# Optimization experiments

Hardware: AMD Instinct MI355X
Metric: run time of the kernel (lower is better)

Reference implementation:

```python
import jax, jax.numpy as jnp
import numpy as np

# Original torch code does the CZT in float64/complex128 explicitly; match it.
jax.config.update("jax_enable_x64", True)

SR = 44100
HOP = 512
MAX_NHAR = 128
REL_WIN = 4
F0_MIN = 40.0  # reconstruction of get_n_fft(): lowest analyzable pitch
N_MAX = int(round(SR / F0_MIN * REL_WIN / 2) * 2)          # 4410: max window size
N_FFT = int(2 ** np.ceil(np.log2(N_MAX)))                  # 8192: used only for padding
L = int(2 ** np.ceil(np.log2(N_MAX + MAX_NHAR - 1)))       # 8192: Bluestein conv length (exact for all frames since L >= n_i + m_i - 1)
N_FRAMES = 1024


def setup_inputs() -> dict:
    key = jax.random.key(0)
    k1, k2 = jax.random.split(key)
    t = N_FRAMES * HOP
    x = jax.random.normal(k1, (t,), dtype=jnp.float32)
    # pitch contour in a realistic 100..400 Hz voice range
    f0 = 100.0 + 300.0 * jax.random.uniform(k2, (N_FRAMES,), dtype=jnp.float32)
    return {"x": x, "f0": f0}


def _sinusoidal_analysis_czt(x, f0):
    # f0: (F,). Vectorized, padded/masked version of the per-frame CZT loop.
    f0 = jnp.clip(f0.astype(jnp.float64), F0_MIN, None)
    F = f0.shape[0]
    nhar = jnp.minimum(jnp.floor(SR / f0 / 2.0), float(MAX_NHAR)).astype(jnp.int32)      # (F,)
    winsize = (jnp.round(SR / f0 * REL_WIN / 2.0) * 2).astype(jnp.int32)                 # (F,) even, <= N_MAX
    pad = N_FFT // 2
    x_pad = jnp.pad(x.astype(jnp.float64), (pad, pad))

    j = jnp.arange(N_MAX)
    start = jnp.arange(F) * HOP + pad                                                    # (F,)
    idx = start[:, None] - winsize[:, None] // 2 + j[None, :]                            # (F, N_MAX)
    frames = x_pad[jnp.clip(idx, 0, x_pad.shape[0] - 1)]
    # torch.blackman_window(n) is periodic: denominator = n
    ratio = j[None, :].astype(jnp.float64) / winsize[:, None].astype(jnp.float64)
    win = 0.42 - 0.5 * jnp.cos(2.0 * np.pi * ratio) + 0.08 * jnp.cos(4.0 * np.pi * ratio)
    valid = j[None, :] < winsize[:, None]
    xw = jnp.where(valid, frames * win, 0.0)                                             # (F, N_MAX) windowed frame, zero-padded

    theta = 2.0 * np.pi * f0 / SR                                                        # (F,) A=exp(+i th), W=exp(-i th)
    jj = j.astype(jnp.float64)
    # gn[j] = x[j] * A^{-j} * W^{j^2/2} = x[j] * exp(-i th (j + j^2/2))
    gphase = -theta[:, None] * (jj[None, :] + 0.5 * jj[None, :] ** 2)
    gn = jnp.zeros((F, L), dtype=jnp.complex128).at[:, :N_MAX].set(xw * jnp.exp(1j * gphase))
    # hn[k] = 1/w[k] = exp(+i th k^2/2) for k < m ; hn[L-j] = exp(+i th j^2/2) for 1 <= j < n
    # (filled for the max ranges; extra entries are never reached because gn is zero beyond winsize)
    kk = jnp.arange(L)
    off = jnp.where(kk < MAX_NHAR, kk, jnp.where(kk > L - N_MAX, L - kk, 0)).astype(jnp.float64)
    hmask = (kk < MAX_NHAR) | (kk > L - N_MAX)
    hn = jnp.where(hmask[None, :], jnp.exp(1j * theta[:, None] * 0.5 * off[None, :] ** 2), 0.0 + 0.0j)
    qn = jnp.fft.ifft(jnp.fft.fft(gn, axis=-1) * jnp.fft.fft(hn, axis=-1), axis=-1)      # (F, L)

    m = jnp.arange(MAX_NHAR).astype(jnp.float64)
    wq = jnp.exp(-1j * theta[:, None] * 0.5 * m[None, :] ** 2)                           # w[:m]
    yn = qn[:, :MAX_NHAR] * wq                                                           # (F, MAX_NHAR)
    yn = 2.381 * yn / (winsize[:, None] // 2 + 1).astype(jnp.float64)
    har_mask = m[None, :] < nhar[:, None].astype(jnp.float64)
    ampl = jnp.where(har_mask, jnp.abs(yn), 0.0).T.astype(jnp.float32)                   # (MAX_NHAR, F)
    phase = jnp.where(har_mask, jnp.angle(yn), 0.0).T.astype(jnp.float32)
    return ampl, phase


def reference(x, f0):
    return _sinusoidal_analysis_czt(x, f0)
```

## Files before the change

kernel.cpp:

```cpp
#include <hip/hip_runtime.h>

#define HOP 512
#define MAX_NHAR 128
#define N_MAX 4410
#define SEGS 8
#define CHUNK_MAX 552
#define PI_D 3.14159265358979323846

__device__ __forceinline__ void frame_params(double f0v, int& w, int& nhar, double& theta) {
    double f0d = f0v < 40.0 ? 40.0 : f0v;
    const double inv = 44100.0 / f0d;
    nhar = (int)fmin(floor(inv * 0.5), 128.0);
    w = 2 * (int)rint(inv * 2.0);
    if (w > N_MAX) w = N_MAX;
    theta = (2.0 * PI_D * f0d) / 44100.0;
}

__device__ __forceinline__ int chunk8_of(int w) {
    return (((w + SEGS - 1) / SEGS) + 7) & ~7;
}

__global__ __launch_bounds__(128) void prep_kernel(
    const float* __restrict__ f0, double* __restrict__ ccos, int F)
{
    const int f = blockIdx.x, k = threadIdx.x;
    int w, nhar; double theta;
    frame_params((double)f0[f], w, nhar, theta);
    ccos[f * MAX_NHAR + k] = cos(theta * (double)(k + 1));
}

__global__ __launch_bounds__(64) void goertzel_kernel(
    const float* __restrict__ x, const float* __restrict__ f0,
    const double* __restrict__ ccos, double2* __restrict__ parts,
    int t, int F)
{
    __shared__ double sm[CHUNK_MAX];
    const int frame = blockIdx.x >> 3;
    const int seg   = blockIdx.x & (SEGS - 1);
    const int lane  = threadIdx.x;

    int w, nhar; double theta;
    frame_params((double)f0[frame], w, nhar, theta);
    const int chunk = chunk8_of(w);
    const int j0 = seg * chunk;
    int lenp = 0;
    if (j0 < w) {
        const int l = w - j0;
        lenp = (l > chunk) ? chunk : ((l + 7) & ~7);
    }

    {
        const double c2pi_invw = (2.0 * PI_D) / (double)w;
        const int base = frame * HOP - (w >> 1) + j0;
        for (int j = lane; j < lenp; j += 64) {
            double outv = 0.0;
            if (j0 + j < w) {
                const int ix = base + j;
                const double val = (ix >= 0 && ix < t) ? (double)x[ix] : 0.0;
                const double c1 = cos(c2pi_invw * (double)(j0 + j));
                const double win = fma(0.16, c1 * c1, 0.34) - 0.5 * c1;
                outv = val * win;
            }
            sm[j] = outv;
        }
    }
    __syncthreads();

    const double Ca = 2.0 * ccos[frame * MAX_NHAR + lane];
    const double Cb = 2.0 * ccos[frame * MAX_NHAR + lane + 64];
    double s1a = 0.0, s2a = 0.0, s1b = 0.0, s2b = 0.0;

    if (nhar > 64) {
        for (int jb = 0; jb < lenp; jb += 8) {
            double xv[8];
            #pragma unroll
            for (int u = 0; u < 8; ++u) xv[u] = sm[jb + u];
            #pragma unroll
            for (int u = 0; u < 8; ++u) {
                const double ta = xv[u] - s2a;
                const double tb = xv[u] - s2b;
                const double na = fma(Ca, s1a, ta);
                const double nb = fma(Cb, s1b, tb);
                s2a = s1a; s1a = na;
                s2b = s1b; s1b = nb;
            }
        }
    } else {
        for (int jb = 0; jb < lenp; jb += 8) {
            double xv[8];
            #pragma unroll
            for (int u = 0; u < 8; ++u) xv[u] = sm[jb + u];
            #pragma unroll
            for (int u = 0; u < 8; ++u) {
                const double ta = xv[u] - s2a;
                const double na = fma(Ca, s1a, ta);
                s2a = s1a; s1a = na;
            }
        }
    }
    double2* p = parts + (size_t)(frame * SEGS + seg) * MAX_NHAR;
    p[lane]      = make_double2(s1a, s2a);
    p[lane + 64] = make_double2(s1b, s2b);
}

__global__ __launch_bounds__(128) void finalize_kernel(
    const float* __restrict__ f0, const double2* __restrict__ parts,
    float* __restrict__ out, int F)
{
    const int frame = blockIdx.x;
    const int tid = threadIdx.x;

    int w, nhar; double theta;
    frame_params((double)f0[frame], w, nhar, theta);
    const int chunk = chunk8_of(w);
    const int slast = (w - 1) / chunk;
    const int endlast = slast * chunk + (((w - slast * chunk) + 7) & ~7);
    const double omega = theta * (double)(tid + 1);

    double sw, cw; sincos(omega, &sw, &cw);
    double sq, cq; sincos(omega * (double)chunk, &sq, &cq);
    double sl, cl; sincos(omega * (double)(endlast - 1), &sl, &cl);

    double Rr = cq * cw + sq * sw, Ri = cq * sw - sq * cw;
    double yr = 0.0, yi = 0.0;
    const double2* p = parts + (size_t)frame * SEGS * MAX_NHAR + tid;
    #pragma unroll
    for (int s = 0; s < SEGS; ++s) {
        const double2 v = p[(size_t)s * MAX_NHAR];
        const double tr = fma(-cw, v.y, v.x);
        const double ti = sw * v.y;
        const double Pr = (s == slast) ? cl : Rr;
        const double Pi = (s == slast) ? -sl : Ri;
        yr = fma(Pr, tr, fma(-Pi, ti, yr));
        yi = fma(Pr, ti, fma( Pi, tr, yi));
        const double nr = Rr * cq + Ri * sq;
        Ri = Ri * cq - Rr * sq; Rr = nr;
    }
    const double scale = 2.381 / (double)((w >> 1) + 1);
    yr *= scale; yi *= scale;

    float ampl = 0.0f, ph = 0.0f;
    if (tid < nhar) {
        ampl = (float)sqrt(yr * yr + yi * yi);
        ph   = (float)atan2(yi, yr);
    }
    out[tid * F + frame] = ampl;
    out[MAX_NHAR * F + tid * F + frame] = ph;
}

__global__ __launch_bounds__(128) void czt_direct_kernel(
    const float* __restrict__ x, const float* __restrict__ f0,
    float* __restrict__ out, int t, int F)
{
    __shared__ double sm[N_MAX];
    const int frame = blockIdx.x;
    const int tid = threadIdx.x;
    int w, nhar; double theta;
    frame_params((double)f0[frame], w, nhar, theta);
    {
        const double invw = 1.0 / (double)w;
        double sa, ca, ss, cs;
        sincos((2.0 * PI_D) * ((double)tid * invw), &sa, &ca);
        sincos((2.0 * PI_D) * (128.0 * invw), &ss, &cs);
        double zr = ca, zi = sa;
        const int base = frame * HOP - (w >> 1);
        for (int j = tid; j < w; j += 128) {
            const int ix = base + j;
            const double val = (ix >= 0 && ix < t) ? (double)x[ix] : 0.0;
            const double c = zr;
            const double win = 0.42 - 0.5 * c + 0.08 * (2.0 * c * c - 1.0);
            sm[j] = val * win;
            const double nzr = zr * cs - zi * ss;
            zi = zr * ss + zi * cs;
            zr = nzr;
        }
    }
    __syncthreads();
    double s, c;
    sincos(theta * (double)(tid + 1), &s, &c);
    const double rr = c, ri = -s;
    const double r2r = rr * rr - ri * ri, r2i = 2.0 * rr * ri;
    const double r4r = r2r * r2r - r2i * r2i, r4i = 2.0 * r2r * r2i;
    const double r3r = r2r * rr - r2i * ri, r3i = r2r * ri + r2i * rr;
    double z0r = 1.0, z0i = 0.0, z1r = rr, z1i = ri;
    double z2r = r2r, z2i = r2i, z3r = r3r, z3i = r3i;
    double a0r = 0, a0i = 0, a1r = 0, a1i = 0, a2r = 0, a2i = 0, a3r = 0, a3i = 0;
    const int w4 = w & ~3;
    for (int j = 0; j < w4; j += 4) {
        const double s0 = sm[j], s1 = sm[j + 1], s2 = sm[j + 2], s3 = sm[j + 3];
        double tr;
        a0r = fma(s0, z0r, a0r); a0i = fma(s0, z0i, a0i);
        tr = z0r * r4r - z0i * r4i; z0i = z0r * r4i + z0i * r4r; z0r = tr;
        a1r = fma(s1, z1r, a1r); a1i = fma(s1, z1i, a1i);
        tr = z1r * r4r - z1i * r4i; z1i = z1r * r4i + z1i * r4r; z1r = tr;
        a2r = fma(s2, z2r, a2r); a2i = fma(s2, z2i, a2i);
        tr = z2r * r4r - z2i * r4i; z2i = z2r * r4i + z2i * r4r; z2r = tr;
        a3r = fma(s3, z3r, a3r); a3i = fma(s3, z3i, a3i);
        tr = z3r * r4r - z3i * r4i; z3i = z3r * r4i + z3i * r4r; z3r = tr;
    }
    if (w4 < w) {
        const double s0 = sm[w4], s1 = sm[w4 + 1];
        a0r = fma(s0, z0r, a0r); a0i = fma(s0, z0i, a0i);
        a1r = fma(s1, z1r, a1r); a1i = fma(s1, z1i, a1i);
    }
    double yr = (a0r + a1r) + (a2r + a3r);
    double yi = (a0i + a1i) + (a2i + a3i);
    const double scale = 2.381 / (double)((w >> 1) + 1);
    yr *= scale; yi *= scale;
    float ampl = 0.0f, ph = 0.0f;
    if (tid < nhar) {
        ampl = (float)sqrt(yr * yr + yi * yi);
        ph   = (float)atan2(yi, yr);
    }
    out[tid * F + frame] = ampl;
    out[MAX_NHAR * F + tid * F + frame] = ph;
}

extern "C" void kernel_launch(void* const* d_in, const int* in_sizes, int n_in,
                              void* d_out, int out_size, void* d_ws, size_t ws_size,
                              hipStream_t stream) {
    const float* x  = (const float*)d_in[0];
    const float* f0 = (const float*)d_in[1];
    float* out = (float*)d_out;
    const int t = in_sizes[0];
    const int F = in_sizes[1];

    const size_t ccos_b  = (size_t)F * MAX_NHAR * sizeof(double);
    const size_t parts_b = (size_t)F * SEGS * MAX_NHAR * sizeof(double2);
    if (ws_size >= ccos_b + parts_b) {
        double*  ccos  = (double*)d_ws;
        double2* parts = (double2*)((char*)d_ws + ccos_b);
        prep_kernel<<<F, 128, 0, stream>>>(f0, ccos, F);
        goertzel_kernel<<<F * SEGS, 64, 0, stream>>>(x, f0, ccos, parts, t, F);
        finalize_kernel<<<F, 128, 0, stream>>>(f0, parts, out, F);
    } else {
        czt_direct_kernel<<<F, 128, 0, stream>>>(x, f0, out, t, F);
    }
}
```

Measured before the change: 83.12 us.

## Pack two Goertzel segments per block and prefetch LDS samples as double2

Each 128-thread block now handles two segments of a frame, one per wavefront, with separate shared buffers, halving the grid size. The block-wide barrier is removed because each wave only reads its own buffer. The recurrence loop software-pipelines shared-memory reads using double2 loads of the next 8 samples while computing the current 8. This aims to cut block-launch overhead and hide LDS latency behind the serial FMA chain, but it relies on intra-wave ordering without an explicit barrier.

```diff
diff --git a/kernel.cpp b/kernel.cpp
--- a/kernel.cpp
+++ b/kernel.cpp
@@ -29,15 +29,16 @@
     ccos[f * MAX_NHAR + k] = cos(theta * (double)(k + 1));
 }
 
-__global__ __launch_bounds__(64) void goertzel_kernel(
+__global__ __launch_bounds__(128) void goertzel_kernel(
     const float* __restrict__ x, const float* __restrict__ f0,
     const double* __restrict__ ccos, double2* __restrict__ parts,
     int t, int F)
 {
-    __shared__ double sm[CHUNK_MAX];
-    const int frame = blockIdx.x >> 3;
-    const int seg   = blockIdx.x & (SEGS - 1);
-    const int lane  = threadIdx.x;
+    __shared__ double sm[2][CHUNK_MAX];
+    const int wave = threadIdx.x >> 6;
+    const int lane = threadIdx.x & 63;
+    const int frame = blockIdx.x >> 2;
+    const int seg   = ((blockIdx.x & 3) << 1) | wave;
 
     int w, nhar; double theta;
     frame_params((double)f0[frame], w, nhar, theta);
@@ -48,6 +49,8 @@
         const int l = w - j0;
         lenp = (l > chunk) ? chunk : ((l + 7) & ~7);
     }
+
+    double* smw = sm[wave];
 
     {
         const double c2pi_invw = (2.0 * PI_D) / (double)w;
@@ -61,40 +64,45 @@
                 const double win = fma(0.16, c1 * c1, 0.34) - 0.5 * c1;
                 outv = val * win;
             }
-            sm[j] = outv;
+            smw[j] = outv;
         }
     }
-    __syncthreads();
 
     const double Ca = 2.0 * ccos[frame * MAX_NHAR + lane];
     const double Cb = 2.0 * ccos[frame * MAX_NHAR + lane + 64];
     double s1a = 0.0, s2a = 0.0, s1b = 0.0, s2b = 0.0;
-
-    if (nhar > 64) {
-        for (int jb = 0; jb < lenp; jb += 8) {
-            double xv[8];
-            #pragma unroll
-            for (int u = 0; u < 8; ++u) xv[u] = sm[jb + u];
-            #pragma unroll
-            for (int u = 0; u < 8; ++u) {
-                const double ta = xv[u] - s2a;
-                const double tb = xv[u] - s2b;
-                const double na = fma(Ca, s1a, ta);
-                const double nb = fma(Cb, s1b, tb);
-                s2a = s1a; s1a = na;
-                s2b = s1b; s1b = nb;
+    const double2* __restrict__ sm2 = (const double2*)smw;
+
+    if (lenp > 0) {
+        double2 c0 = sm2[0], c1 = sm2[1], c2 = sm2[2], c3 = sm2[3];
+        if (nhar > 64) {
+            for (int jb = 0; jb < lenp; jb += 8) {
+                const int nb = (jb + 8 < lenp) ? ((jb + 8) >> 1) : 0;
+                const double2 n0 = sm2[nb], n1 = sm2[nb + 1], n2 = sm2[nb + 2], n3 = sm2[nb + 3];
+                double xv[8] = {c0.x, c0.y, c1.x, c1.y, c2.x, c2.y, c3.x, c3.y};
+                #pragma unroll
+                for (int u = 0; u < 8; ++u) {
+                    const double ta = xv[u] - s2a;
+                    const double tb = xv[u] - s2b;
+                    const double na = fma(Ca, s1a, ta);
+                    const double nb2 = fma(Cb, s1b, tb);
+                    s2a = s1a; s1a = na;
+                    s2b = s1b; s1b = nb2;
+                }
+                c0 = n0; c1 = n1; c2 = n2; c3 = n3;
             }
-        }
-    } else {
-        for (int jb = 0; jb < lenp; jb += 8) {
-            double xv[8];
-            #pragma unroll
-            for (int u = 0; u < 8; ++u) xv[u] = sm[jb + u];
-            #pragma unroll
-            for (int u = 0; u < 8; ++u) {
-                const double ta = xv[u] - s2a;
-                const double na = fma(Ca, s1a, ta);
-                s2a = s1a; s1a = na;
+        } else {
+            for (int jb = 0; jb < lenp; jb += 8) {
+                const int nb = (jb + 8 < lenp) ? ((jb + 8) >> 1) : 0;
+                const double2 n0 = sm2[nb], n1 = sm2[nb + 1], n2 = sm2[nb + 2], n3 = sm2[nb + 3];
+                double xv[8] = {c0.x, c0.y, c1.x, c1.y, c2.x, c2.y, c3.x, c3.y};
+                #pragma unroll
+                for (int u = 0; u < 8; ++u) {
+                    const double ta = xv[u] - s2a;
+                    const double na = fma(Ca, s1a, ta);
+                    s2a = s1a; s1a = na;
+                }
+                c0 = n0; c1 = n1; c2 = n2; c3 = n3;
             }
         }
     }
@@ -231,7 +239,7 @@
         double*  ccos  = (double*)d_ws;
         double2* parts = (double2*)((char*)d_ws + ccos_b);
         prep_kernel<<<F, 128, 0, stream>>>(f0, ccos, F);
-        goertzel_kernel<<<F * SEGS, 64, 0, stream>>>(x, f0, ccos, parts, t, F);
+        goertzel_kernel<<<F * SEGS / 2, 128, 0, stream>>>(x, f0, ccos, parts, t, F);
         finalize_kernel<<<F, 128, 0, stream>>>(f0, parts, out, F);
     } else {
         czt_direct_kernel<<<F, 128, 0, stream>>>(x, f0, out, t, F);
```

Measured after the change: 83.12 us. About the same (-0.0%).
